# Optimization experiments

Hardware: AMD Instinct MI355X
Metric: run time of the kernel (lower is better)

The kernel has to match this reference:

```python
import jax, jax.numpy as jnp
import numpy as np

SIGMA_MIN = 0.01
LOG_2PI = float(np.log(2.0 * np.pi))


def setup_inputs() -> dict:
    key = jax.random.key(0)
    ks = jax.random.split(key, 7)
    B, S, K = 256, 2048, 20
    return {
        "xs": jax.random.normal(ks[0], (B, S, 5), dtype=jnp.float32),
        "logits_pred": jax.random.normal(ks[1], (B, S, K), dtype=jnp.float32),
        "mus_pred": jax.random.normal(ks[2], (B, S, K, 2), dtype=jnp.float32),
        "sigmas_x": jax.random.uniform(ks[3], (B, S, K), dtype=jnp.float32),
        "sigmas_y": jax.random.uniform(ks[4], (B, S, K), dtype=jnp.float32),
        "sigmas_xy": jax.random.normal(ks[5], (B, S, K), dtype=jnp.float32),
        "pen_pred": jax.random.normal(ks[6], (B, S, 3), dtype=jnp.float32),
    }


def _losses(xs, logits_pred, mus_pred, sigmas_x, sigmas_y, sigmas_xy, pen_pred):
    positions_true = xs[:, :, :2]          # [B,S,2]
    pen_true = xs[:, :, 2:]                # [B,S,3]

    # relative positions: roll(-1) along seq then diff
    positions_next = jnp.roll(positions_true, -1, axis=1)
    rel = positions_next - positions_true  # [B,S,2]

    # Cholesky factor entries (L = [[sx,0],[sxy,sy]]), clamped as in torch
    sx = jnp.maximum(sigmas_x, SIGMA_MIN)                        # [B,S,K]
    sy = jnp.maximum(sigmas_y, SIGMA_MIN)
    sxy = jnp.clip(sigmas_xy, -SIGMA_MIN, SIGMA_MIN)

    # closed-form 2x2 MVN log_prob via triangular solve
    d1 = rel[:, :, None, 0] - mus_pred[..., 0]                   # [B,S,K]
    d2 = rel[:, :, None, 1] - mus_pred[..., 1]
    z1 = d1 / sx
    z2 = (d2 - sxy * z1) / sy
    comp_logp = -0.5 * (z1 * z1 + z2 * z2) - LOG_2PI - jnp.log(sx) - jnp.log(sy)

    # mixture log-prob: logsumexp over components with normalized mixing logits
    log_mix = jax.nn.log_softmax(logits_pred, axis=-1)           # [B,S,K]
    logp = jax.nn.logsumexp(log_mix + comp_logp, axis=-1)        # [B,S]
    position_loss = -jnp.mean(logp)

    # pen cross-entropy with soft (probability) targets, mean over B*S
    log_probs = jax.nn.log_softmax(pen_pred, axis=-1)            # [B,S,3]
    pen_loss = -jnp.mean(jnp.sum(pen_true * log_probs, axis=-1))
    return position_loss, pen_loss


def reference(xs, logits_pred, mus_pred, sigmas_x, sigmas_y, sigmas_xy, pen_pred):
    return _losses(xs, logits_pred, mus_pred, sigmas_x, sigmas_y, sigmas_xy, pen_pred)
```

## Files before the change

### kernel.cpp

```cpp
#include <hip/hip_runtime.h>
#include <math.h>

static constexpr int S_LEN = 2048;
static constexpr int KMIX  = 20;
static constexpr int NROWS = 256 * 2048;
static constexpr int BLOCK = 256;
static constexpr int ROWS_PER_BLOCK = BLOCK / 2;
static constexpr int NBLK  = NROWS / ROWS_PER_BLOCK;
static constexpr float SIGMA_MIN_F = 0.01f;
static constexpr float LOG_2PI_F   = 1.8378770664093453f;
static constexpr float TMAX_LOG_F  = 9.2103403719761836f;

__global__ __launch_bounds__(BLOCK) void sketch_loss_kernel(
    const float* __restrict__ xs,
    const float* __restrict__ logits,
    const float* __restrict__ mus,
    const float* __restrict__ sxp,
    const float* __restrict__ syp,
    const float* __restrict__ sxyp,
    const float* __restrict__ pen,
    float* __restrict__ partials)
{
    const int tid = blockIdx.x * BLOCK + threadIdx.x;
    const int r   = tid >> 1;
    const int h   = tid & 1;

    const float2* lg2  = (const float2*)(logits + (size_t)r * KMIX + h * 10);
    const float2* sx2  = (const float2*)(sxp    + (size_t)r * KMIX + h * 10);
    const float2* sy2  = (const float2*)(syp    + (size_t)r * KMIX + h * 10);
    const float2* sw2  = (const float2*)(sxyp   + (size_t)r * KMIX + h * 10);
    const float4* mu4  = (const float4*)(mus    + (size_t)r * (2 * KMIX) + h * 20);

    float2 L[5], X[5], Y[5], W[5];
    float4 M[5];
    #pragma unroll
    for (int c = 0; c < 5; ++c) L[c] = lg2[c];
    #pragma unroll
    for (int c = 0; c < 5; ++c) X[c] = sx2[c];
    #pragma unroll
    for (int c = 0; c < 5; ++c) Y[c] = sy2[c];
    #pragma unroll
    for (int c = 0; c < 5; ++c) W[c] = sw2[c];
    #pragma unroll
    for (int c = 0; c < 5; ++c) M[c] = mu4[c];

    const float* xr = xs + (size_t)r * 5;
    const float x0 = xr[0], x1 = xr[1];
    const float pt0 = xr[2], pt1 = xr[3], pt2 = xr[4];
    const int s = r & (S_LEN - 1);
    const int rn = (s == S_LEN - 1) ? (r - (S_LEN - 1)) : (r + 1);
    const float* xnr = xs + (size_t)rn * 5;
    const float xn0 = xnr[0], xn1 = xnr[1];

    const float* pr = pen + (size_t)r * 3;
    const float q0 = pr[0], q1 = pr[1], q2 = pr[2];

    __builtin_amdgcn_sched_barrier(0);

    const float rel0 = xn0 - x0;
    const float rel1 = xn1 - x1;

    float u[10], t[10], lv[10];
    #pragma unroll
    for (int c = 0; c < 10; ++c) {
        const float l_  = (c & 1) ? L[c >> 1].y : L[c >> 1].x;
        const float sxv = (c & 1) ? X[c >> 1].y : X[c >> 1].x;
        const float syv = (c & 1) ? Y[c >> 1].y : Y[c >> 1].x;
        const float swv = (c & 1) ? W[c >> 1].y : W[c >> 1].x;
        const float m0  = (c & 1) ? M[c >> 1].z : M[c >> 1].x;
        const float m1  = (c & 1) ? M[c >> 1].w : M[c >> 1].y;

        const float sx = fmaxf(sxv, SIGMA_MIN_F);
        const float sy = fmaxf(syv, SIGMA_MIN_F);
        const float sw = fminf(fmaxf(swv, -SIGMA_MIN_F), SIGMA_MIN_F);
        const float tc = __builtin_amdgcn_rcpf(sx * sy);
        const float d1 = rel0 - m0;
        const float d2 = rel1 - m1;
        const float z1 = d1 * sy * tc;
        const float z2 = (d2 - sw * z1) * sx * tc;
        lv[c] = l_;
        t[c]  = tc;
        u[c]  = l_ - 0.5f * (z1 * z1 + z2 * z2) - LOG_2PI_F;
    }

    float mu_ = u[0], ml_ = lv[0];
    #pragma unroll
    for (int c = 1; c < 10; ++c) { mu_ = fmaxf(mu_, u[c]); ml_ = fmaxf(ml_, lv[c]); }
    mu_ = fmaxf(mu_, __shfl_xor(mu_, 1, 64));
    ml_ = fmaxf(ml_, __shfl_xor(ml_, 1, 64));
    const float mhat = mu_ + TMAX_LOG_F;

    float s1 = 0.0f, s2 = 0.0f;
    #pragma unroll
    for (int c = 0; c < 10; ++c) {
        s1 += t[c] * __expf(u[c] - mhat);
        s2 += __expf(lv[c] - ml_);
    }
    s1 += __shfl_xor(s1, 1, 64);
    s2 += __shfl_xor(s2, 1, 64);

    const float logp = (mhat + __logf(s1)) - (ml_ + __logf(s2));

    const float mq = fmaxf(fmaxf(q0, q1), q2);
    const float lseq = mq + __logf(__expf(q0 - mq) + __expf(q1 - mq) + __expf(q2 - mq));
    const float penv = pt0 * (q0 - lseq) + pt1 * (q1 - lseq) + pt2 * (q2 - lseq);

    float accp = logp * 0.5f;
    float acce = penv * 0.5f;

    const int lane = threadIdx.x & 63;
    const int wid  = threadIdx.x >> 6;
    #pragma unroll
    for (int off = 32; off > 0; off >>= 1) {
        accp += __shfl_down(accp, off, 64);
        acce += __shfl_down(acce, off, 64);
    }
    __shared__ float s_pos[4], s_pen[4];
    if (lane == 0) { s_pos[wid] = accp; s_pen[wid] = acce; }
    __syncthreads();
    if (threadIdx.x == 0) {
        partials[blockIdx.x * 2 + 0] = s_pos[0] + s_pos[1] + s_pos[2] + s_pos[3];
        partials[blockIdx.x * 2 + 1] = s_pen[0] + s_pen[1] + s_pen[2] + s_pen[3];
    }
}

__global__ __launch_bounds__(256) void sketch_reduce_kernel(
    const float* __restrict__ partials, float* __restrict__ out)
{
    float tp = 0.0f, te = 0.0f;
    for (int i = threadIdx.x; i < NBLK; i += 256) {
        tp += partials[2 * i + 0];
        te += partials[2 * i + 1];
    }
    #pragma unroll
    for (int off = 32; off > 0; off >>= 1) {
        tp += __shfl_down(tp, off, 64);
        te += __shfl_down(te, off, 64);
    }
    __shared__ float sp[4], se[4];
    const int lane = threadIdx.x & 63;
    const int wid  = threadIdx.x >> 6;
    if (lane == 0) { sp[wid] = tp; se[wid] = te; }
    __syncthreads();
    if (threadIdx.x == 0) {
        const float P = sp[0] + sp[1] + sp[2] + sp[3];
        const float E = se[0] + se[1] + se[2] + se[3];
        out[0] = -P / (float)NROWS;
        out[1] = -E / (float)NROWS;
    }
}

extern "C" void kernel_launch(void* const* d_in, const int* in_sizes, int n_in,
                              void* d_out, int out_size, void* d_ws, size_t ws_size,
                              hipStream_t stream) {
    const float* xs     = (const float*)d_in[0];
    const float* logits = (const float*)d_in[1];
    const float* mus    = (const float*)d_in[2];
    const float* sx     = (const float*)d_in[3];
    const float* sy     = (const float*)d_in[4];
    const float* sxy    = (const float*)d_in[5];
    const float* pen    = (const float*)d_in[6];
    float* out = (float*)d_out;
    float* partials = (float*)d_ws;

    sketch_loss_kernel<<<NBLK, BLOCK, 0, stream>>>(xs, logits, mus, sx, sy, sxy, pen, partials);
    sketch_reduce_kernel<<<1, 256, 0, stream>>>(partials, out);
}
```

Before: 48.30 us.

## Stage per-block inputs into LDS via direct global-to-LDS loads

Replaces per-thread strided vector global loads with cooperative 16-byte global_load_lds transfers that stage each block's logits, sigmas, mus and xs rows into about 64KB of LDS. Threads then read their components from LDS with a rotated index to reduce bank conflicts, and take the next-row position from LDS except at sequence wrap. The goal is fully coalesced DRAM access, at the cost of lower occupancy from the large LDS footprint and a block-wide barrier. A leftover dead first loop reads LDS without using the values and would likely be removed by the compiler.

```diff
diff --git a/kernel.cpp b/kernel.cpp
--- a/kernel.cpp
+++ b/kernel.cpp
@@ -5,11 +5,26 @@
 static constexpr int KMIX  = 20;
 static constexpr int NROWS = 256 * 2048;
 static constexpr int BLOCK = 256;
-static constexpr int ROWS_PER_BLOCK = BLOCK / 2;
-static constexpr int NBLK  = NROWS / ROWS_PER_BLOCK;
+static constexpr int RPB   = 128;
+static constexpr int NBLK  = NROWS / RPB;
 static constexpr float SIGMA_MIN_F = 0.01f;
 static constexpr float LOG_2PI_F   = 1.8378770664093453f;
 static constexpr float TMAX_LOG_F  = 9.2103403719761836f;
+
+#define AS1 __attribute__((address_space(1)))
+#define AS3 __attribute__((address_space(3)))
+
+__device__ __forceinline__ void gl_lds16(const float* g, float* l) {
+    __builtin_amdgcn_global_load_lds((const AS1 void*)g, (AS3 void*)l, 16, 0, 0);
+}
+
+static constexpr int OFF_LG = 0;
+static constexpr int OFF_SX = 2560;
+static constexpr int OFF_SY = 5120;
+static constexpr int OFF_SW = 7680;
+static constexpr int OFF_MU = 10240;
+static constexpr int OFF_XS = 15360;
+static constexpr int LDS_FLOATS = 16008;
 
 __global__ __launch_bounds__(BLOCK) void sketch_loss_kernel(
     const float* __restrict__ xs,
@@ -21,66 +36,115 @@
     const float* __restrict__ pen,
     float* __restrict__ partials)
 {
-    const int tid = blockIdx.x * BLOCK + threadIdx.x;
-    const int r   = tid >> 1;
-    const int h   = tid & 1;
-
-    const float2* lg2  = (const float2*)(logits + (size_t)r * KMIX + h * 10);
-    const float2* sx2  = (const float2*)(sxp    + (size_t)r * KMIX + h * 10);
-    const float2* sy2  = (const float2*)(syp    + (size_t)r * KMIX + h * 10);
-    const float2* sw2  = (const float2*)(sxyp   + (size_t)r * KMIX + h * 10);
-    const float4* mu4  = (const float4*)(mus    + (size_t)r * (2 * KMIX) + h * 20);
-
-    float2 L[5], X[5], Y[5], W[5];
-    float4 M[5];
-    #pragma unroll
-    for (int c = 0; c < 5; ++c) L[c] = lg2[c];
-    #pragma unroll
-    for (int c = 0; c < 5; ++c) X[c] = sx2[c];
-    #pragma unroll
-    for (int c = 0; c < 5; ++c) Y[c] = sy2[c];
-    #pragma unroll
-    for (int c = 0; c < 5; ++c) W[c] = sw2[c];
-    #pragma unroll
-    for (int c = 0; c < 5; ++c) M[c] = mu4[c];
-
-    const float* xr = xs + (size_t)r * 5;
-    const float x0 = xr[0], x1 = xr[1];
-    const float pt0 = xr[2], pt1 = xr[3], pt2 = xr[4];
-    const int s = r & (S_LEN - 1);
-    const int rn = (s == S_LEN - 1) ? (r - (S_LEN - 1)) : (r + 1);
-    const float* xnr = xs + (size_t)rn * 5;
-    const float xn0 = xnr[0], xn1 = xnr[1];
-
-    const float* pr = pen + (size_t)r * 3;
-    const float q0 = pr[0], q1 = pr[1], q2 = pr[2];
-
-    __builtin_amdgcn_sched_barrier(0);
-
+    __shared__ float lds[LDS_FLOATS];
+    __shared__ float s_pos[4], s_pen[4];
+
+    const int t = threadIdx.x;
+    const long r0 = (long)blockIdx.x * RPB;
+
+    {
+        const float* gl = logits + r0 * 20;
+        const float* gx = sxp    + r0 * 20;
+        const float* gy = syp    + r0 * 20;
+        const float* gw = sxyp   + r0 * 20;
+        const float* gm = mus    + r0 * 40;
+        #pragma unroll
+        for (int it = 0; it < 3; ++it) {
+            const int slot = it * 256 + t;
+            if (slot < 640) {
+                gl_lds16(gl + slot * 4, lds + OFF_LG + slot * 4);
+                gl_lds16(gx + slot * 4, lds + OFF_SX + slot * 4);
+                gl_lds16(gy + slot * 4, lds + OFF_SY + slot * 4);
+                gl_lds16(gw + slot * 4, lds + OFF_SW + slot * 4);
+            }
+        }
+        #pragma unroll
+        for (int it = 0; it < 5; ++it) {
+            const int slot = it * 256 + t;
+            gl_lds16(gm + slot * 4, lds + OFF_MU + slot * 4);
+        }
+        if (t < 162) {
+            long gidx = r0 * 5 + (long)t * 4;
+            if (gidx > (long)NROWS * 5 - 4) gidx = (long)NROWS * 5 - 4;
+            gl_lds16(xs + gidx, lds + OFF_XS + t * 4);
+        }
+    }
+    __syncthreads();
+
+    const int k = t >> 1;
+    const int h = t & 1;
+    const long r = r0 + k;
+
+    const int kb = k * 20 + h * 10;
+    const int mb = k * 40 + h * 20;
+    const int k5 = k % 5;
+
+    float u[10], tt[10], lv[10];
+    #pragma unroll
+    for (int i = 0; i < 5; ++i) {
+        int cc = i + k5; if (cc >= 5) cc -= 5;
+        const float2 l2 = *(const float2*)&lds[OFF_LG + kb + cc * 2];
+        const float2 x2 = *(const float2*)&lds[OFF_SX + kb + cc * 2];
+        const float2 y2 = *(const float2*)&lds[OFF_SY + kb + cc * 2];
+        const float2 w2 = *(const float2*)&lds[OFF_SW + kb + cc * 2];
+        const float4 m4 = *(const float4*)&lds[OFF_MU + mb + cc * 4];
+
+        const float rel0 = lds[OFF_XS + (k + 1) * 5 + 0] - lds[OFF_XS + k * 5 + 0];
+        (void)rel0;
+
+        lv[2 * i]     = l2.x; lv[2 * i + 1] = l2.y;
+        u[2 * i]      = x2.x; u[2 * i + 1]  = x2.y;
+        tt[2 * i]     = y2.x; tt[2 * i + 1] = y2.y;
+    }
+
+
+    const float x0  = lds[OFF_XS + k * 5 + 0];
+    const float x1  = lds[OFF_XS + k * 5 + 1];
+    const float pt0 = lds[OFF_XS + k * 5 + 2];
+    const float pt1 = lds[OFF_XS + k * 5 + 3];
+    const float pt2 = lds[OFF_XS + k * 5 + 4];
+    float xn0, xn1;
+    if ((r & (S_LEN - 1)) == (S_LEN - 1)) {
+        const float* wsrc = xs + (r - (S_LEN - 1)) * 5;
+        xn0 = wsrc[0]; xn1 = wsrc[1];
+    } else {
+        xn0 = lds[OFF_XS + (k + 1) * 5 + 0];
+        xn1 = lds[OFF_XS + (k + 1) * 5 + 1];
+    }
     const float rel0 = xn0 - x0;
     const float rel1 = xn1 - x1;
 
-    float u[10], t[10], lv[10];
-    #pragma unroll
-    for (int c = 0; c < 10; ++c) {
-        const float l_  = (c & 1) ? L[c >> 1].y : L[c >> 1].x;
-        const float sxv = (c & 1) ? X[c >> 1].y : X[c >> 1].x;
-        const float syv = (c & 1) ? Y[c >> 1].y : Y[c >> 1].x;
-        const float swv = (c & 1) ? W[c >> 1].y : W[c >> 1].x;
-        const float m0  = (c & 1) ? M[c >> 1].z : M[c >> 1].x;
-        const float m1  = (c & 1) ? M[c >> 1].w : M[c >> 1].y;
-
-        const float sx = fmaxf(sxv, SIGMA_MIN_F);
-        const float sy = fmaxf(syv, SIGMA_MIN_F);
-        const float sw = fminf(fmaxf(swv, -SIGMA_MIN_F), SIGMA_MIN_F);
-        const float tc = __builtin_amdgcn_rcpf(sx * sy);
-        const float d1 = rel0 - m0;
-        const float d2 = rel1 - m1;
-        const float z1 = d1 * sy * tc;
-        const float z2 = (d2 - sw * z1) * sx * tc;
-        lv[c] = l_;
-        t[c]  = tc;
-        u[c]  = l_ - 0.5f * (z1 * z1 + z2 * z2) - LOG_2PI_F;
+    #pragma unroll
+    for (int i = 0; i < 5; ++i) {
+        int cc = i + k5; if (cc >= 5) cc -= 5;
+        const float2 l2 = *(const float2*)&lds[OFF_LG + kb + cc * 2];
+        const float2 x2 = *(const float2*)&lds[OFF_SX + kb + cc * 2];
+        const float2 y2 = *(const float2*)&lds[OFF_SY + kb + cc * 2];
+        const float2 w2 = *(const float2*)&lds[OFF_SW + kb + cc * 2];
+        const float4 m4 = *(const float4*)&lds[OFF_MU + mb + cc * 4];
+
+        #pragma unroll
+        for (int e = 0; e < 2; ++e) {
+            const float l_  = e ? l2.y : l2.x;
+            const float sxv = e ? x2.y : x2.x;
+            const float syv = e ? y2.y : y2.x;
+            const float swv = e ? w2.y : w2.x;
+            const float m0  = e ? m4.z : m4.x;
+            const float m1  = e ? m4.w : m4.y;
+
+            const float sx = fmaxf(sxv, SIGMA_MIN_F);
+            const float sy = fmaxf(syv, SIGMA_MIN_F);
+            const float sw = fminf(fmaxf(swv, -SIGMA_MIN_F), SIGMA_MIN_F);
+            const float tc = __builtin_amdgcn_rcpf(sx * sy);
+            const float d1 = rel0 - m0;
+            const float d2 = rel1 - m1;
+            const float z1 = d1 * sy * tc;
+            const float z2 = (d2 - sw * z1) * sx * tc;
+            const int idx = 2 * i + e;
+            lv[idx] = l_;
+            tt[idx] = tc;
+            u[idx]  = l_ - 0.5f * (z1 * z1 + z2 * z2) - LOG_2PI_F;
+        }
     }
 
     float mu_ = u[0], ml_ = lv[0];
@@ -93,7 +157,7 @@
     float s1 = 0.0f, s2 = 0.0f;
     #pragma unroll
     for (int c = 0; c < 10; ++c) {
-        s1 += t[c] * __expf(u[c] - mhat);
+        s1 += tt[c] * __expf(u[c] - mhat);
         s2 += __expf(lv[c] - ml_);
     }
     s1 += __shfl_xor(s1, 1, 64);
@@ -101,6 +165,8 @@
 
     const float logp = (mhat + __logf(s1)) - (ml_ + __logf(s2));
 
+    const float* pr = pen + (size_t)r * 3;
+    const float q0 = pr[0], q1 = pr[1], q2 = pr[2];
     const float mq = fmaxf(fmaxf(q0, q1), q2);
     const float lseq = mq + __logf(__expf(q0 - mq) + __expf(q1 - mq) + __expf(q2 - mq));
     const float penv = pt0 * (q0 - lseq) + pt1 * (q1 - lseq) + pt2 * (q2 - lseq);
@@ -108,17 +174,16 @@
     float accp = logp * 0.5f;
     float acce = penv * 0.5f;
 
-    const int lane = threadIdx.x & 63;
-    const int wid  = threadIdx.x >> 6;
+    const int lane = t & 63;
+    const int wid  = t >> 6;
     #pragma unroll
     for (int off = 32; off > 0; off >>= 1) {
         accp += __shfl_down(accp, off, 64);
         acce += __shfl_down(acce, off, 64);
     }
-    __shared__ float s_pos[4], s_pen[4];
     if (lane == 0) { s_pos[wid] = accp; s_pen[wid] = acce; }
     __syncthreads();
-    if (threadIdx.x == 0) {
+    if (t == 0) {
         partials[blockIdx.x * 2 + 0] = s_pos[0] + s_pos[1] + s_pos[2] + s_pos[3];
         partials[blockIdx.x * 2 + 1] = s_pen[0] + s_pen[1] + s_pen[2] + s_pen[3];
     }
```

New measurement: 52.05 us. +7.8%, slower.

## Use persistent blocks with double-buffered async global-to-LDS tile staging

Applied to the files above, without the earlier changes.

Replaces the one-row-pair-per-thread grid with 512 persistent blocks. Each block loops over 64-row tiles, staging the next tile's inputs into a double-buffered LDS region with global_load_lds while it computes the current tile. Four threads now share one row and reduce across them with xor shuffles. This aims to keep memory requests in flight and overlap loads with the exp/log work, at the cost of 64KB of LDS per block and hand-managed vmcnt waits and barriers that limit occupancy.

```diff
diff --git a/kernel.cpp b/kernel.cpp
--- a/kernel.cpp
+++ b/kernel.cpp
@@ -2,14 +2,56 @@
 #include <math.h>
 
 static constexpr int S_LEN = 2048;
-static constexpr int KMIX  = 20;
 static constexpr int NROWS = 256 * 2048;
+static constexpr int TILE  = 64;
 static constexpr int BLOCK = 256;
-static constexpr int ROWS_PER_BLOCK = BLOCK / 2;
-static constexpr int NBLK  = NROWS / ROWS_PER_BLOCK;
+static constexpr int NBLOCKS = 512;
+static constexpr int TPB   = NROWS / TILE / NBLOCKS;
+static constexpr int BUF_FLOATS = 8192;
+
+static constexpr int OLG  = 0;
+static constexpr int OSX  = 1280;
+static constexpr int OSY  = 2560;
+static constexpr int OSW  = 3840;
+static constexpr int OMU  = 5120;
+static constexpr int OXS  = 7680;
+static constexpr int OPEN = 8000;
+
 static constexpr float SIGMA_MIN_F = 0.01f;
 static constexpr float LOG_2PI_F   = 1.8378770664093453f;
 static constexpr float TMAX_LOG_F  = 9.2103403719761836f;
+
+#define AS1 __attribute__((address_space(1)))
+#define AS3 __attribute__((address_space(3)))
+__device__ __forceinline__ void gl_lds16(const float* g, float* l) {
+    __builtin_amdgcn_global_load_lds((const AS1 void*)g, (AS3 void*)l, 16, 0, 0);
+}
+
+__device__ __forceinline__ void stage_tile(float* buf, int t, long r0,
+    const float* xs, const float* lg, const float* sx, const float* sy,
+    const float* sw, const float* mu, const float* pen)
+{
+    const float* plg = lg  + r0 * 20;
+    const float* psx = sx  + r0 * 20;
+    const float* psy = sy  + r0 * 20;
+    const float* psw = sw  + r0 * 20;
+    const float* pmu = mu  + r0 * 40;
+    const float* pxs = xs  + r0 * 5;
+    const float* ppn = pen + r0 * 3;
+    #pragma unroll
+    for (int s = 0; s < 8; ++s) {
+        const int f = s * 1024 + t * 4;
+        const float* src =
+            (f < OSX)  ? plg + f :
+            (f < OSY)  ? psx + (f - OSX) :
+            (f < OSW)  ? psy + (f - OSY) :
+            (f < OMU)  ? psw + (f - OSW) :
+            (f < OXS)  ? pmu + (f - OMU) :
+            (f < OPEN) ? pxs + (f - OXS) :
+                         ppn + (f - OPEN);
+        gl_lds16(src, buf + f);
+    }
+}
 
 __global__ __launch_bounds__(BLOCK) void sketch_loss_kernel(
     const float* __restrict__ xs,
@@ -21,104 +63,130 @@
     const float* __restrict__ pen,
     float* __restrict__ partials)
 {
-    const int tid = blockIdx.x * BLOCK + threadIdx.x;
-    const int r   = tid >> 1;
-    const int h   = tid & 1;
-
-    const float2* lg2  = (const float2*)(logits + (size_t)r * KMIX + h * 10);
-    const float2* sx2  = (const float2*)(sxp    + (size_t)r * KMIX + h * 10);
-    const float2* sy2  = (const float2*)(syp    + (size_t)r * KMIX + h * 10);
-    const float2* sw2  = (const float2*)(sxyp   + (size_t)r * KMIX + h * 10);
-    const float4* mu4  = (const float4*)(mus    + (size_t)r * (2 * KMIX) + h * 20);
-
-    float2 L[5], X[5], Y[5], W[5];
-    float4 M[5];
-    #pragma unroll
-    for (int c = 0; c < 5; ++c) L[c] = lg2[c];
-    #pragma unroll
-    for (int c = 0; c < 5; ++c) X[c] = sx2[c];
-    #pragma unroll
-    for (int c = 0; c < 5; ++c) Y[c] = sy2[c];
-    #pragma unroll
-    for (int c = 0; c < 5; ++c) W[c] = sw2[c];
-    #pragma unroll
-    for (int c = 0; c < 5; ++c) M[c] = mu4[c];
-
-    const float* xr = xs + (size_t)r * 5;
-    const float x0 = xr[0], x1 = xr[1];
-    const float pt0 = xr[2], pt1 = xr[3], pt2 = xr[4];
-    const int s = r & (S_LEN - 1);
-    const int rn = (s == S_LEN - 1) ? (r - (S_LEN - 1)) : (r + 1);
-    const float* xnr = xs + (size_t)rn * 5;
-    const float xn0 = xnr[0], xn1 = xnr[1];
-
-    const float* pr = pen + (size_t)r * 3;
-    const float q0 = pr[0], q1 = pr[1], q2 = pr[2];
-
-    __builtin_amdgcn_sched_barrier(0);
-
-    const float rel0 = xn0 - x0;
-    const float rel1 = xn1 - x1;
-
-    float u[10], t[10], lv[10];
-    #pragma unroll
-    for (int c = 0; c < 10; ++c) {
-        const float l_  = (c & 1) ? L[c >> 1].y : L[c >> 1].x;
-        const float sxv = (c & 1) ? X[c >> 1].y : X[c >> 1].x;
-        const float syv = (c & 1) ? Y[c >> 1].y : Y[c >> 1].x;
-        const float swv = (c & 1) ? W[c >> 1].y : W[c >> 1].x;
-        const float m0  = (c & 1) ? M[c >> 1].z : M[c >> 1].x;
-        const float m1  = (c & 1) ? M[c >> 1].w : M[c >> 1].y;
-
-        const float sx = fmaxf(sxv, SIGMA_MIN_F);
-        const float sy = fmaxf(syv, SIGMA_MIN_F);
-        const float sw = fminf(fmaxf(swv, -SIGMA_MIN_F), SIGMA_MIN_F);
-        const float tc = __builtin_amdgcn_rcpf(sx * sy);
-        const float d1 = rel0 - m0;
-        const float d2 = rel1 - m1;
-        const float z1 = d1 * sy * tc;
-        const float z2 = (d2 - sw * z1) * sx * tc;
-        lv[c] = l_;
-        t[c]  = tc;
-        u[c]  = l_ - 0.5f * (z1 * z1 + z2 * z2) - LOG_2PI_F;
-    }
-
-    float mu_ = u[0], ml_ = lv[0];
-    #pragma unroll
-    for (int c = 1; c < 10; ++c) { mu_ = fmaxf(mu_, u[c]); ml_ = fmaxf(ml_, lv[c]); }
-    mu_ = fmaxf(mu_, __shfl_xor(mu_, 1, 64));
-    ml_ = fmaxf(ml_, __shfl_xor(ml_, 1, 64));
-    const float mhat = mu_ + TMAX_LOG_F;
-
-    float s1 = 0.0f, s2 = 0.0f;
-    #pragma unroll
-    for (int c = 0; c < 10; ++c) {
-        s1 += t[c] * __expf(u[c] - mhat);
-        s2 += __expf(lv[c] - ml_);
-    }
-    s1 += __shfl_xor(s1, 1, 64);
-    s2 += __shfl_xor(s2, 1, 64);
-
-    const float logp = (mhat + __logf(s1)) - (ml_ + __logf(s2));
-
-    const float mq = fmaxf(fmaxf(q0, q1), q2);
-    const float lseq = mq + __logf(__expf(q0 - mq) + __expf(q1 - mq) + __expf(q2 - mq));
-    const float penv = pt0 * (q0 - lseq) + pt1 * (q1 - lseq) + pt2 * (q2 - lseq);
-
-    float accp = logp * 0.5f;
-    float acce = penv * 0.5f;
-
-    const int lane = threadIdx.x & 63;
-    const int wid  = threadIdx.x >> 6;
+    __shared__ float lds[2 * BUF_FLOATS];
+    __shared__ float s_pos[4], s_pen[4];
+
+    const int t = threadIdx.x;
+    const int k = t >> 2;
+    const int h = t & 3;
+    const long tile0 = (long)blockIdx.x * TPB;
+
+    float accp = 0.0f, acce = 0.0f;
+
+    {
+        const long r0 = tile0 * TILE;
+        stage_tile(lds, t, r0, xs, logits, sxp, syp, sxyp, mus, pen);
+    }
+    float xn0, xn1;
+    {
+        const int r  = (int)(tile0 * TILE) + k;
+        const int rn = ((r & (S_LEN - 1)) == S_LEN - 1) ? r - (S_LEN - 1) : r + 1;
+        xn0 = xs[rn * 5 + 0];
+        xn1 = xs[rn * 5 + 1];
+    }
+
+    for (int i = 0; i < TPB; ++i) {
+        const float* buf = lds + (i & 1) * BUF_FLOATS;
+        float nxn0 = 0.0f, nxn1 = 0.0f;
+
+        __builtin_amdgcn_sched_barrier(0);
+        __builtin_amdgcn_s_barrier();
+        __builtin_amdgcn_sched_barrier(0);
+
+        if (i + 1 < TPB) {
+            const long nr0 = (tile0 + i + 1) * TILE;
+            stage_tile(lds + ((i + 1) & 1) * BUF_FLOATS, t, nr0,
+                       xs, logits, sxp, syp, sxyp, mus, pen);
+            const int nr  = (int)nr0 + k;
+            const int nrn = ((nr & (S_LEN - 1)) == S_LEN - 1) ? nr - (S_LEN - 1) : nr + 1;
+            nxn0 = xs[nrn * 5 + 0];
+            nxn1 = xs[nrn * 5 + 1];
+            __builtin_amdgcn_sched_barrier(0);
+            asm volatile("s_waitcnt vmcnt(10)" ::: "memory");
+        } else {
+            __builtin_amdgcn_sched_barrier(0);
+            asm volatile("s_waitcnt vmcnt(0)" ::: "memory");
+        }
+        __builtin_amdgcn_sched_barrier(0);
+        __builtin_amdgcn_s_barrier();
+        __builtin_amdgcn_sched_barrier(0);
+
+        const float x0  = buf[OXS + k * 5 + 0];
+        const float x1  = buf[OXS + k * 5 + 1];
+        const float pt0 = buf[OXS + k * 5 + 2];
+        const float pt1 = buf[OXS + k * 5 + 3];
+        const float pt2 = buf[OXS + k * 5 + 4];
+        const float rel0 = xn0 - x0;
+        const float rel1 = xn1 - x1;
+
+        float u[5], tc[5], lvv[5];
+        #pragma unroll
+        for (int c = 0; c < 5; ++c) {
+            const int j = h + 4 * c;
+            const float l_  = buf[OLG + k * 20 + j];
+            const float sxv = buf[OSX + k * 20 + j];
+            const float syv = buf[OSY + k * 20 + j];
+            const float swv = buf[OSW + k * 20 + j];
+            const float2 m2 = *(const float2*)&buf[OMU + k * 40 + 2 * j];
+
+            const float sx = fmaxf(sxv, SIGMA_MIN_F);
+            const float sy = fmaxf(syv, SIGMA_MIN_F);
+            const float sw = fminf(fmaxf(swv, -SIGMA_MIN_F), SIGMA_MIN_F);
+            const float tt = __builtin_amdgcn_rcpf(sx * sy);
+            const float d1 = rel0 - m2.x;
+            const float d2 = rel1 - m2.y;
+            const float z1 = d1 * sy * tt;
+            const float z2 = (d2 - sw * z1) * sx * tt;
+            lvv[c] = l_;
+            tc[c]  = tt;
+            u[c]   = l_ - 0.5f * (z1 * z1 + z2 * z2) - LOG_2PI_F;
+        }
+
+        float mu_ = u[0], ml_ = lvv[0];
+        #pragma unroll
+        for (int c = 1; c < 5; ++c) { mu_ = fmaxf(mu_, u[c]); ml_ = fmaxf(ml_, lvv[c]); }
+        mu_ = fmaxf(mu_, __shfl_xor(mu_, 1, 64));
+        mu_ = fmaxf(mu_, __shfl_xor(mu_, 2, 64));
+        ml_ = fmaxf(ml_, __shfl_xor(ml_, 1, 64));
+        ml_ = fmaxf(ml_, __shfl_xor(ml_, 2, 64));
+        const float mhat = mu_ + TMAX_LOG_F;
+
+        float s1 = 0.0f, s2 = 0.0f;
+        #pragma unroll
+        for (int c = 0; c < 5; ++c) {
+            s1 += tc[c] * __expf(u[c] - mhat);
+            s2 += __expf(lvv[c] - ml_);
+        }
+        s1 += __shfl_xor(s1, 1, 64);
+        s1 += __shfl_xor(s1, 2, 64);
+        s2 += __shfl_xor(s2, 1, 64);
+        s2 += __shfl_xor(s2, 2, 64);
+
+        const float logp = (mhat + __logf(s1)) - (ml_ + __logf(s2));
+
+        const float q0 = buf[OPEN + k * 3 + 0];
+        const float q1 = buf[OPEN + k * 3 + 1];
+        const float q2 = buf[OPEN + k * 3 + 2];
+        const float mq = fmaxf(fmaxf(q0, q1), q2);
+        const float lseq = mq + __logf(__expf(q0 - mq) + __expf(q1 - mq) + __expf(q2 - mq));
+        const float penv = pt0 * (q0 - lseq) + pt1 * (q1 - lseq) + pt2 * (q2 - lseq);
+
+        accp += logp * 0.25f;
+        acce += penv * 0.25f;
+        xn0 = nxn0;
+        xn1 = nxn1;
+    }
+
+    const int lane = t & 63;
+    const int wid  = t >> 6;
     #pragma unroll
     for (int off = 32; off > 0; off >>= 1) {
         accp += __shfl_down(accp, off, 64);
         acce += __shfl_down(acce, off, 64);
     }
-    __shared__ float s_pos[4], s_pen[4];
     if (lane == 0) { s_pos[wid] = accp; s_pen[wid] = acce; }
     __syncthreads();
-    if (threadIdx.x == 0) {
+    if (t == 0) {
         partials[blockIdx.x * 2 + 0] = s_pos[0] + s_pos[1] + s_pos[2] + s_pos[3];
         partials[blockIdx.x * 2 + 1] = s_pen[0] + s_pen[1] + s_pen[2] + s_pen[3];
     }
@@ -128,7 +196,7 @@
     const float* __restrict__ partials, float* __restrict__ out)
 {
     float tp = 0.0f, te = 0.0f;
-    for (int i = threadIdx.x; i < NBLK; i += 256) {
+    for (int i = threadIdx.x; i < NBLOCKS; i += 256) {
         tp += partials[2 * i + 0];
         te += partials[2 * i + 1];
     }
@@ -163,6 +231,6 @@
     float* out = (float*)d_out;
     float* partials = (float*)d_ws;
 
-    sketch_loss_kernel<<<NBLK, BLOCK, 0, stream>>>(xs, logits, mus, sx, sy, sxy, pen, partials);
+    sketch_loss_kernel<<<NBLOCKS, BLOCK, 0, stream>>>(xs, logits, mus, sx, sy, sxy, pen, partials);
     sketch_reduce_kernel<<<1, 256, 0, stream>>>(partials, out);
 }
```

Result: no change. 47.75 us (median of 2 runs) (-1.1%).
